# Kernel tuning notes

Measured on AMD Instinct MI355X. Metric: run time of the kernel, lower is better.

The kernel has to match this reference:

```python
import jax, jax.numpy as jnp
import numpy as np

B, M, K = 32768, 8192, 16
EPS = 1e-5  # torch BatchNorm1d default


def _bn_relu(x, g, b):
    # training-mode batch norm (biased variance), matching torch BatchNorm1d forward
    m = x.mean(0)
    v = x.var(0)
    return jax.nn.relu(g * (x - m) * jax.lax.rsqrt(v + EPS) + b)


def _forward(pos, mc, mv, w1, b1, w2, b2, w3, b3, w4, b4, w5, b5, w6, b6,
             g1, be1, g2, be2, g3, be3, g4, be4, g5, be5, k):
    # squared pairwise distances [B, M]; same ordering as L2 norm used by torch.sort
    d2 = (pos * pos).sum(1, keepdims=True) + (mc * mc).sum(1)[None, :] - 2.0 * (pos @ mc.T)
    _, idx = jax.lax.top_k(-d2, k)                     # k nearest indices [B, k]
    nb = jnp.concatenate([mc[idx], mv[idx]], axis=-1)  # [B, k, 4] = (coord, value) per neighbor
    knn_feat = jnp.concatenate([pos, nb.reshape(pos.shape[0], k * 4)], axis=1)  # [B, 2+4k]
    x = _bn_relu(knn_feat @ w1 + b1, g1, be1)
    x = _bn_relu(x @ w2 + b2, g2, be2)
    x = _bn_relu(x @ w3 + b3, g3, be3)
    x = _bn_relu(x @ w4 + b4, g4, be4)
    x = _bn_relu(x @ w5 + b5, g5, be5)  # dropout = identity (eval mode)
    x = x @ w6 + b6
    return x, knn_feat


def setup_inputs() -> dict:
    key = jax.random.key(0)
    ks = jax.random.split(key, 32)
    d_in = 2 + K * 4
    dims = [(d_in, 128), (128, 256), (256, 512), (512, 128), (128, 64), (64, 2)]
    inp = {
        "pos": jax.random.normal(ks[0], (B, 2), jnp.float32),
        "measure_coords": jax.random.normal(ks[1], (M, 2), jnp.float32),
        "measure_vals": jax.random.normal(ks[2], (M, 2), jnp.float32),
    }
    for i, (fi, fo) in enumerate(dims, 1):
        inp[f"w{i}"] = jax.random.normal(ks[2 + 2 * i], (fi, fo), jnp.float32) / np.float32(np.sqrt(fi))
        inp[f"b{i}"] = jnp.zeros((fo,), jnp.float32)
    for i, n in enumerate([128, 256, 512, 128, 64], 1):
        inp[f"g{i}"] = jnp.ones((n,), jnp.float32)
        inp[f"be{i}"] = jnp.zeros((n,), jnp.float32)
    inp["k"] = K
    return inp


def reference(pos, measure_coords, measure_vals, w1, b1, w2, b2, w3, b3, w4, b4,
              w5, b5, w6, b6, g1, be1, g2, be2, g3, be3, g4, be4, g5, be5, k):
    return _forward(pos, measure_coords, measure_vals, w1, b1, w2, b2, w3, b3, w4,
                    b4, w5, b5, w6, b6, g1, be1, g2, be2, g3, be3, g4, be4, g5, be5, k)
```

## Files before the change

### kernel.cpp

```cpp
#include <hip/hip_runtime.h>

typedef unsigned short u16;
typedef unsigned int   u32;
typedef __attribute__((ext_vector_type(8))) short bf16x8;
typedef __attribute__((ext_vector_type(4))) float f32x4;

#define B_ROWS 32768
#define EPS_BN 1e-5f

__device__ __forceinline__ u16 f2bf(float f) {
  u32 u = __float_as_uint(f);
  u32 r = (u + 0x7FFFu + ((u >> 16) & 1u)) >> 16;
  return (u16)r;
}
__device__ __forceinline__ float bf2f(u16 h) {
  return __uint_as_float(((u32)h) << 16);
}

__device__ __forceinline__ float dcalc(float px, float py, float sp, float mx, float my) {
#pragma clang fp contract(off)
  float sm   = mx * mx + my * my;
  float pm   = px * mx;
  float dot  = __builtin_fmaf(py, my, pm);
  float spsm = sp + sm;
  return spsm - 2.0f * dot;
}
__device__ __forceinline__ float dcalc2(float px, float py, float sp, float mx, float my,
                                        float sm) {
#pragma clang fp contract(off)
  float pm   = px * mx;
  float dot  = __builtin_fmaf(py, my, pm);
  float spsm = sp + sm;
  return spsm - 2.0f * dot;
}
__device__ __forceinline__ float smcalc(float mx, float my) {
#pragma clang fp contract(off)
  return mx * mx + my * my;
}
__device__ __forceinline__ float spcalc(float px, float py) {
#pragma clang fp contract(off)
  return px * px + py * py;
}
#define MED3 __builtin_amdgcn_fmed3f

__global__ __launch_bounds__(256, 4)
void knn_kernel(const float2* __restrict__ pos, const float2* __restrict__ mc,
                const float2* __restrict__ mv, float* __restrict__ knn_out,
                u16* __restrict__ X0)
{
  __shared__ float tv[32 * 130];
  __shared__ float tstS[32];
  __shared__ int   qcnt[32];

  const int t = threadIdx.x;
  const int g = t >> 6;
  const int s = t & 63;
  const int q0 = blockIdx.x * 32;

  float px[8], py[8], sp[8];
#pragma unroll
  for (int j = 0; j < 8; ++j) {
    float2 p = pos[q0 + g * 8 + j];
    px[j] = p.x; py[j] = p.y; sp[j] = spcalc(p.x, p.y);
  }

  const float4* mc4 = (const float4*)mc;
  const int b4 = s * 64;
  const int basePt = s * 128;

  float z0[8], z1[8];
#pragma unroll
  for (int j = 0; j < 8; ++j) { z0[j] = __builtin_inff(); z1[j] = __builtin_inff(); }

  float4 cur = mc4[b4];
  for (int i = 0; i < 64; ++i) {
    float4 nxt = mc4[b4 + ((i + 1) & 63)];
    float smA = smcalc(cur.x, cur.y);
    float smB = smcalc(cur.z, cur.w);
#pragma unroll
    for (int j = 0; j < 8; ++j) {
      float dA = dcalc2(px[j], py[j], sp[j], cur.x, cur.y, smA);
      z1[j] = MED3(z0[j], dA, z1[j]); z0[j] = fminf(z0[j], dA);
      float dB = dcalc2(px[j], py[j], sp[j], cur.z, cur.w, smB);
      z1[j] = MED3(z0[j], dB, z1[j]); z0[j] = fminf(z0[j], dB);
    }
    cur = nxt;
  }
#pragma unroll
  for (int j = 0; j < 8; ++j) {
    tv[(g * 8 + j) * 130 + s * 2 + 0] = z0[j];
    tv[(g * 8 + j) * 130 + s * 2 + 1] = z1[j];
  }
  __syncthreads();

  if (t < 32) {
    float ch[16];
#pragma unroll
    for (int j = 0; j < 16; ++j) ch[j] = __builtin_inff();
    for (int k = 0; k < 128; ++k) {
      float v = tv[t * 130 + k];
#pragma unroll
      for (int j = 15; j >= 1; --j) ch[j] = MED3(ch[j-1], v, ch[j]);
      ch[0] = fminf(ch[0], v);
    }
    tstS[t] = ch[15];
    qcnt[t] = 0;
  }
  __syncthreads();
  float Tq[8];
#pragma unroll
  for (int j = 0; j < 8; ++j) Tq[j] = tstS[g * 8 + j];
  __syncthreads();

  u16* qcand = (u16*)tv;
  for (int i = 0; i < 64; ++i) {
    float4 c2 = mc4[b4 + i];
    float smA = smcalc(c2.x, c2.y);
    float smB = smcalc(c2.z, c2.w);
    const int idxA = basePt + 2 * i;
#pragma unroll
    for (int j = 0; j < 8; ++j) {
      float dA = dcalc2(px[j], py[j], sp[j], c2.x, c2.y, smA);
      if (dA <= Tq[j]) {
        int o = atomicAdd(&qcnt[g * 8 + j], 1);
        if (o < 64) qcand[(g * 8 + j) * 64 + o] = (u16)idxA;
      }
      float dB = dcalc2(px[j], py[j], sp[j], c2.z, c2.w, smB);
      if (dB <= Tq[j]) {
        int o = atomicAdd(&qcnt[g * 8 + j], 1);
        if (o < 64) qcand[(g * 8 + j) * 64 + o] = (u16)(idxA + 1);
      }
    }
  }
  __syncthreads();

  if (t < 32) {
    const int q = q0 + t;
    float2 p = pos[q];
    const float sq = spcalc(p.x, p.y);
    int cnt = qcnt[t]; if (cnt > 64) cnt = 64;
    float fd[16]; int fi[16];
#pragma unroll
    for (int j = 0; j < 16; ++j) { fd[j] = __builtin_inff(); fi[j] = 0x7fffffff; }
    for (int j = 0; j < cnt; ++j) {
      int ci = qcand[t * 64 + j];
      float2 m = mc[ci];
      float d = dcalc(p.x, p.y, sq, m.x, m.y);
      bool cc = (d < fd[15]) || (d == fd[15] && ci < fi[15]);
      if (cc) {
#pragma unroll
        for (int k = 15; k >= 1; --k) {
          bool cm = (d < fd[k-1]) || (d == fd[k-1] && ci < fi[k-1]);
          if (cc) {
            if (cm) { fd[k] = fd[k-1]; fi[k] = fi[k-1]; }
            else    { fd[k] = d;       fi[k] = ci;      }
          }
          cc = cm;
        }
        if (cc) { fd[0] = d; fi[0] = ci; }
      }
    }
    float* orow = knn_out + (size_t)q * 66;
    u16*   xrow = X0 + (size_t)q * 96;
    orow[0] = p.x; orow[1] = p.y;
    xrow[0] = f2bf(p.x); xrow[1] = f2bf(p.y);
#pragma unroll
    for (int j = 0; j < 16; ++j) {
      int ci = fi[j];
      float2 m = mc[ci], v = mv[ci];
      orow[2 + 4*j + 0] = m.x; orow[2 + 4*j + 1] = m.y;
      orow[2 + 4*j + 2] = v.x; orow[2 + 4*j + 3] = v.y;
      xrow[2 + 4*j + 0] = f2bf(m.x); xrow[2 + 4*j + 1] = f2bf(m.y);
      xrow[2 + 4*j + 2] = f2bf(v.x); xrow[2 + 4*j + 3] = f2bf(v.y);
    }
#pragma unroll
    for (int c = 66; c < 96; ++c) xrow[c] = 0;
  }
}

__global__ __launch_bounds__(256)
void prep_wt_all(const float* __restrict__ w1, const float* __restrict__ w2,
                 const float* __restrict__ w3, const float* __restrict__ w4,
                 const float* __restrict__ w5,
                 u16* __restrict__ wt1, u16* __restrict__ wt2, u16* __restrict__ wt3,
                 u16* __restrict__ wt4, u16* __restrict__ wt5)
{
  const int l = blockIdx.y;
  const float* w; u16* wt; int K, N, Kp;
  if (l == 0)      { w = w1; wt = wt1; K = 66;  N = 128; Kp = 96;  }
  else if (l == 1) { w = w2; wt = wt2; K = 128; N = 256; Kp = 128; }
  else if (l == 2) { w = w3; wt = wt3; K = 256; N = 512; Kp = 256; }
  else if (l == 3) { w = w4; wt = wt4; K = 512; N = 128; Kp = 512; }
  else             { w = w5; wt = wt5; K = 128; N = 64;  Kp = 128; }
  int i = blockIdx.x * 256 + threadIdx.x;
  if (i >= N * Kp) return;
  int n = i / Kp, kp = i - n * Kp;
  float v = (kp < K) ? w[(size_t)kp * N + n] : 0.0f;
  wt[i] = f2bf(v);
}

template<int BN, bool FUSE>
__global__ __launch_bounds__(256)
void gemm_bn_kernel(const u16* __restrict__ X, int Kw,
                    const u16* __restrict__ WT,
                    const float* __restrict__ bias,
                    const float* __restrict__ psum, const float* __restrict__ psq,
                    const float* __restrict__ gw,   const float* __restrict__ bw,
                    u16* __restrict__ Z, int N,
                    float* __restrict__ csum, float* __restrict__ csq)
{
  constexpr int BM = 128;
  constexpr int AST = 40;
  __shared__ u16 Ash[BM * AST];
  __shared__ u16 Bsh[BN * AST];
  __shared__ float redS[4][BN];
  __shared__ float redQ[4][BN];
  __shared__ float scA[512];
  __shared__ float ttA[512];

  const int t = threadIdx.x;
  const int wave = t >> 6;
  const int lane = t & 63;
  const int lr = lane & 15;
  const int qd = lane >> 4;
  const int m0 = blockIdx.x * BM;
  const int n0 = blockIdx.y * BN;

  if (FUSE) {
    const float invB = 1.0f / 32768.0f;
    for (int c = t; c < Kw; c += 256) {
      float mean = psum[c] * invB;
      float var  = __fmaf_rn(-mean, mean, psq[c] * invB);
      float sc   = gw[c] * rsqrtf(var + EPS_BN);
      scA[c] = sc;
      ttA[c] = __fmaf_rn(-mean, sc, bw[c]);
    }
    __syncthreads();
  }

  f32x4 acc[2][BN / 16];
#pragma unroll
  for (int a = 0; a < 2; ++a)
#pragma unroll
    for (int b = 0; b < BN / 16; ++b) {
      acc[a][b][0] = 0.f; acc[a][b][1] = 0.f; acc[a][b][2] = 0.f; acc[a][b][3] = 0.f;
    }

  const int sr = t >> 2;
  const int sk = (t & 3) * 8;

  for (int k0 = 0; k0 < Kw; k0 += 32) {
#pragma unroll
    for (int rr = 0; rr < 2; ++rr) {
      int r = sr + rr * 64;
      uint4 g = *(const uint4*)(&X[(size_t)(m0 + r) * Kw + k0 + sk]);
      if (FUSE) {
        u32 w[4] = {g.x, g.y, g.z, g.w};
        u32 o[4];
#pragma unroll
        for (int e = 0; e < 4; ++e) {
          int kk = k0 + sk + 2 * e;
          float lo = bf2f((u16)(w[e] & 0xffffu));
          float hi = bf2f((u16)(w[e] >> 16));
          float yl = fmaxf(__fmaf_rn(lo, scA[kk],     ttA[kk]),     0.0f);
          float yh = fmaxf(__fmaf_rn(hi, scA[kk + 1], ttA[kk + 1]), 0.0f);
          o[e] = (u32)f2bf(yl) | ((u32)f2bf(yh) << 16);
        }
        g.x = o[0]; g.y = o[1]; g.z = o[2]; g.w = o[3];
      }
      *(uint4*)(&Ash[r * AST + sk]) = g;
    }
    if (BN == 128) {
#pragma unroll
      for (int rr = 0; rr < 2; ++rr) {
        int n = sr + rr * 64;
        *(uint4*)(&Bsh[n * AST + sk]) =
            *(const uint4*)(&WT[(size_t)(n0 + n) * Kw + k0 + sk]);
      }
    } else {
      int n = sr;
      *(uint4*)(&Bsh[n * AST + sk]) =
          *(const uint4*)(&WT[(size_t)(n0 + n) * Kw + k0 + sk]);
    }
    __syncthreads();
    bf16x8 af0 = *(const bf16x8*)(&Ash[(wave * 32 + lr) * AST + qd * 8]);
    bf16x8 af1 = *(const bf16x8*)(&Ash[(wave * 32 + 16 + lr) * AST + qd * 8]);
#pragma unroll
    for (int ct = 0; ct < BN / 16; ++ct) {
      bf16x8 bfr = *(const bf16x8*)(&Bsh[(ct * 16 + lr) * AST + qd * 8]);
      acc[0][ct] = __builtin_amdgcn_mfma_f32_16x16x32_bf16(af0, bfr, acc[0][ct], 0, 0, 0);
      acc[1][ct] = __builtin_amdgcn_mfma_f32_16x16x32_bf16(af1, bfr, acc[1][ct], 0, 0, 0);
    }
    __syncthreads();
  }

#pragma unroll
  for (int ct = 0; ct < BN / 16; ++ct) {
    int cg = n0 + ct * 16 + lr;
    float bv = bias[cg];
    float s = 0.f, sqv = 0.f;
#pragma unroll
    for (int rt = 0; rt < 2; ++rt) {
#pragma unroll
      for (int r = 0; r < 4; ++r) {
        float z = acc[rt][ct][r] + bv;
        int row = m0 + wave * 32 + rt * 16 + qd * 4 + r;
        Z[(size_t)row * N + cg] = f2bf(z);
        s += z;
        sqv = __fmaf_rn(z, z, sqv);
      }
    }
    s   += __shfl_xor(s, 16);   s   += __shfl_xor(s, 32);
    sqv += __shfl_xor(sqv, 16); sqv += __shfl_xor(sqv, 32);
    if (qd == 0) { redS[wave][ct * 16 + lr] = s; redQ[wave][ct * 16 + lr] = sqv; }
  }
  __syncthreads();
  if (t < BN) {
    float s  = redS[0][t] + redS[1][t] + redS[2][t] + redS[3][t];
    float sv = redQ[0][t] + redQ[1][t] + redQ[2][t] + redQ[3][t];
    atomicAdd(&csum[n0 + t], s);
    atomicAdd(&csq[n0 + t], sv);
  }
}

__global__ __launch_bounds__(256)
void gemv6_kernel(const u16* __restrict__ Z5, const float* __restrict__ w6,
                  const float* __restrict__ b6,
                  const float* __restrict__ psum, const float* __restrict__ psq,
                  const float* __restrict__ gw,   const float* __restrict__ bw,
                  float* __restrict__ out)
{
  __shared__ float wsh[128];
  __shared__ float scs[64];
  __shared__ float tts[64];
  const int t = threadIdx.x;
  if (t < 128) wsh[t] = w6[t];
  if (t < 64) {
    const float invB = 1.0f / 32768.0f;
    float mean = psum[t] * invB;
    float var  = __fmaf_rn(-mean, mean, psq[t] * invB);
    float sc   = gw[t] * rsqrtf(var + EPS_BN);
    scs[t] = sc;
    tts[t] = __fmaf_rn(-mean, sc, bw[t]);
  }
  __syncthreads();
  const int q = blockIdx.x * 256 + t;
  const uint4* xv = (const uint4*)(Z5 + (size_t)q * 64);
  float a0 = 0.f, a1 = 0.f;
#pragma unroll
  for (int cc = 0; cc < 8; ++cc) {
    uint4 pk = xv[cc];
    u32 u[4] = {pk.x, pk.y, pk.z, pk.w};
#pragma unroll
    for (int uu = 0; uu < 4; ++uu) {
      int k = cc * 8 + uu * 2;
      float z0 = bf2f((u16)(u[uu] & 0xffffu));
      float z1 = bf2f((u16)(u[uu] >> 16));
      float x0 = fmaxf(__fmaf_rn(z0, scs[k],     tts[k]),     0.0f);
      float x1 = fmaxf(__fmaf_rn(z1, scs[k + 1], tts[k + 1]), 0.0f);
      x0 = bf2f(f2bf(x0));
      x1 = bf2f(f2bf(x1));
      a0 = __fmaf_rn(x0, wsh[2 * k + 0], a0);
      a1 = __fmaf_rn(x0, wsh[2 * k + 1], a1);
      a0 = __fmaf_rn(x1, wsh[2 * k + 2], a0);
      a1 = __fmaf_rn(x1, wsh[2 * k + 3], a1);
    }
  }
  float2 o; o.x = a0 + b6[0]; o.y = a1 + b6[1];
  ((float2*)out)[q] = o;
}

extern "C" void kernel_launch(void* const* d_in, const int* in_sizes, int n_in,
                              void* d_out, int out_size, void* d_ws, size_t ws_size,
                              hipStream_t stream)
{
  const float2* pos = (const float2*)d_in[0];
  const float2* mc  = (const float2*)d_in[1];
  const float2* mv  = (const float2*)d_in[2];
  const float* w1 = (const float*)d_in[3];  const float* b1 = (const float*)d_in[4];
  const float* w2 = (const float*)d_in[5];  const float* b2 = (const float*)d_in[6];
  const float* w3 = (const float*)d_in[7];  const float* b3 = (const float*)d_in[8];
  const float* w4 = (const float*)d_in[9];  const float* b4 = (const float*)d_in[10];
  const float* w5 = (const float*)d_in[11]; const float* b5 = (const float*)d_in[12];
  const float* w6 = (const float*)d_in[13]; const float* b6 = (const float*)d_in[14];
  const float* g1 = (const float*)d_in[15]; const float* be1 = (const float*)d_in[16];
  const float* g2 = (const float*)d_in[17]; const float* be2 = (const float*)d_in[18];
  const float* g3 = (const float*)d_in[19]; const float* be3 = (const float*)d_in[20];
  const float* g4 = (const float*)d_in[21]; const float* be4 = (const float*)d_in[22];
  const float* g5 = (const float*)d_in[23]; const float* be5 = (const float*)d_in[24];

  char* ws = (char*)d_ws;
  u16* X0   = (u16*)(ws + 0);
  u16* ZA   = (u16*)(ws + 6291456);
  u16* ZB   = (u16*)(ws + 39845888);
  u16* WT1  = (u16*)(ws + 73400320);
  u16* WT2  = (u16*)(ws + 73424896);
  u16* WT3  = (u16*)(ws + 73490432);
  u16* WT4  = (u16*)(ws + 73752576);
  u16* WT5  = (u16*)(ws + 73883648);
  float* stats = (float*)(ws + 73900032);
  float* s1 = stats;        float* s2 = stats + 128;  float* s3 = stats + 384;
  float* s4 = stats + 896;  float* s5 = stats + 1024;
  float* sqb = stats + 1088;
  float* q1 = sqb;          float* q2 = sqb + 128;    float* q3 = sqb + 384;
  float* q4 = sqb + 896;    float* q5 = sqb + 1024;

  float* outX = (float*)d_out;
  float* outK = outX + 2 * B_ROWS;

  hipMemsetAsync(stats, 0, 2176 * sizeof(float), stream);
  prep_wt_all<<<dim3(512, 5), 256, 0, stream>>>(w1, w2, w3, w4, w5, WT1, WT2, WT3, WT4, WT5);
  knn_kernel<<<dim3(1024), 256, 0, stream>>>(pos, mc, mv, outK, X0);

  gemm_bn_kernel<64, false><<<dim3(256, 2), 256, 0, stream>>>(
      X0, 96, WT1, b1, nullptr, nullptr, nullptr, nullptr, ZA, 128, s1, q1);
  gemm_bn_kernel<64, true><<<dim3(256, 4), 256, 0, stream>>>(
      ZA, 128, WT2, b2, s1, q1, g1, be1, ZB, 256, s2, q2);
  gemm_bn_kernel<64, true><<<dim3(256, 8), 256, 0, stream>>>(
      ZB, 256, WT3, b3, s2, q2, g2, be2, ZA, 512, s3, q3);
  gemm_bn_kernel<64, true><<<dim3(256, 2), 256, 0, stream>>>(
      ZA, 512, WT4, b4, s3, q3, g3, be3, ZB, 128, s4, q4);
  gemm_bn_kernel<64, true><<<dim3(256, 1), 256, 0, stream>>>(
      ZB, 128, WT5, b5, s4, q4, g4, be4, ZA, 64, s5, q5);
  gemv6_kernel<<<dim3(128), 256, 0, stream>>>(ZA, w6, b6, s5, q5, g5, be5, outX);

  (void)in_sizes; (void)n_in; (void)out_size; (void)ws_size;
}
```

Measured before the change: 360.1 us.

## Rescan only slices whose local min passes the threshold, compacted via ballot

The second candidate-collection pass no longer rescans every slice of measurement points for every query. A ballot over each lane's local minimum marks only the (query, slice) pairs that can hold a point under the top-k threshold, and those pairs are spread across lanes to be rescanned. This cuts the redundant distance evaluations and atomics in the second pass, at the cost of bit-select and per-lane branching work. Separately, the distance formula now uses an explicit fma for the final term, which may change rounding relative to the reference ordering.

```diff
diff --git a/kernel.cpp b/kernel.cpp
--- a/kernel.cpp
+++ b/kernel.cpp
@@ -23,7 +23,7 @@
   float pm   = px * mx;
   float dot  = __builtin_fmaf(py, my, pm);
   float spsm = sp + sm;
-  return spsm - 2.0f * dot;
+  return __builtin_fmaf(dot, -2.0f, spsm);
 }
 __device__ __forceinline__ float dcalc2(float px, float py, float sp, float mx, float my,
                                         float sm) {
@@ -31,7 +31,7 @@
   float pm   = px * mx;
   float dot  = __builtin_fmaf(py, my, pm);
   float spsm = sp + sm;
-  return spsm - 2.0f * dot;
+  return __builtin_fmaf(dot, -2.0f, spsm);
 }
 __device__ __forceinline__ float smcalc(float mx, float my) {
 #pragma clang fp contract(off)
@@ -42,6 +42,29 @@
   return px * px + py * py;
 }
 #define MED3 __builtin_amdgcn_fmed3f
+
+__device__ __forceinline__ int nth_set_bit(unsigned long long m, int n) {
+  u32 w = (u32)m;
+  int base = 0;
+  int c = __popc(w);
+  if (n >= c) { n -= c; w = (u32)(m >> 32); base = 32; }
+  int p = __popc(w & 0xFFFFu); if (n >= p) { n -= p; w >>= 16; base += 16; }
+  p = __popc(w & 0xFFu);       if (n >= p) { n -= p; w >>= 8;  base += 8; }
+  p = __popc(w & 0xFu);        if (n >= p) { n -= p; w >>= 4;  base += 4; }
+  p = __popc(w & 0x3u);        if (n >= p) { n -= p; w >>= 2;  base += 2; }
+  p = (int)(w & 1u);           if (n >= p) { base += 1; }
+  return base;
+}
+
+__device__ __forceinline__ float sel8(const float a[8], int j) {
+  float x01 = (j & 1) ? a[1] : a[0];
+  float x23 = (j & 1) ? a[3] : a[2];
+  float x45 = (j & 1) ? a[5] : a[4];
+  float x67 = (j & 1) ? a[7] : a[6];
+  float xl  = (j & 2) ? x23 : x01;
+  float xh  = (j & 2) ? x67 : x45;
+  return (j & 4) ? xh : xl;
+}
 
 __global__ __launch_bounds__(256, 4)
 void knn_kernel(const float2* __restrict__ pos, const float2* __restrict__ mc,
@@ -66,7 +89,6 @@
 
   const float4* mc4 = (const float4*)mc;
   const int b4 = s * 64;
-  const int basePt = s * 128;
 
   float z0[8], z1[8];
 #pragma unroll
@@ -88,8 +110,8 @@
   }
 #pragma unroll
   for (int j = 0; j < 8; ++j) {
-    tv[(g * 8 + j) * 130 + s * 2 + 0] = z0[j];
-    tv[(g * 8 + j) * 130 + s * 2 + 1] = z1[j];
+    float2 zz; zz.x = z0[j]; zz.y = z1[j];
+    *(float2*)(&tv[(g * 8 + j) * 130 + s * 2]) = zz;
   }
   __syncthreads();
 
@@ -112,23 +134,43 @@
   for (int j = 0; j < 8; ++j) Tq[j] = tstS[g * 8 + j];
   __syncthreads();
 
+  unsigned long long am[8];
+#pragma unroll
+  for (int j = 0; j < 8; ++j) am[j] = __ballot(z0[j] <= Tq[j]);
+  int total = 0;
+#pragma unroll
+  for (int j = 0; j < 8; ++j) total += __popcll(am[j]);
+
   u16* qcand = (u16*)tv;
-  for (int i = 0; i < 64; ++i) {
-    float4 c2 = mc4[b4 + i];
-    float smA = smcalc(c2.x, c2.y);
-    float smB = smcalc(c2.z, c2.w);
-    const int idxA = basePt + 2 * i;
-#pragma unroll
-    for (int j = 0; j < 8; ++j) {
-      float dA = dcalc2(px[j], py[j], sp[j], c2.x, c2.y, smA);
-      if (dA <= Tq[j]) {
-        int o = atomicAdd(&qcnt[g * 8 + j], 1);
-        if (o < 64) qcand[(g * 8 + j) * 64 + o] = (u16)idxA;
-      }
-      float dB = dcalc2(px[j], py[j], sp[j], c2.z, c2.w, smB);
-      if (dB <= Tq[j]) {
-        int o = atomicAdd(&qcnt[g * 8 + j], 1);
-        if (o < 64) qcand[(g * 8 + j) * 64 + o] = (u16)(idxA + 1);
+  for (int t0 = s; t0 < total; t0 += 64) {
+    int rem = t0, jq = 0, sl = -1;
+#pragma unroll
+    for (int jj = 0; jj < 8; ++jj) {
+      if (sl < 0) {
+        int c = __popcll(am[jj]);
+        if (rem < c) { sl = nth_set_bit(am[jj], rem); jq = jj; }
+        else rem -= c;
+      }
+    }
+    float qx = sel8(px, jq), qy = sel8(py, jq);
+    float qs = sel8(sp, jq), qT = sel8(Tq, jq);
+    const int qrow = g * 8 + jq;
+    const int bpt = sl * 128;
+    const float4* mbase = mc4 + sl * 64;
+#pragma unroll 4
+    for (int i = 0; i < 64; ++i) {
+      float4 c2 = mbase[i];
+      float smA = smcalc(c2.x, c2.y);
+      float smB = smcalc(c2.z, c2.w);
+      float dA = dcalc2(qx, qy, qs, c2.x, c2.y, smA);
+      float dB = dcalc2(qx, qy, qs, c2.z, c2.w, smB);
+      if (dA <= qT) {
+        int o = atomicAdd(&qcnt[qrow], 1);
+        if (o < 64) qcand[qrow * 64 + o] = (u16)(bpt + 2 * i);
+      }
+      if (dB <= qT) {
+        int o = atomicAdd(&qcnt[qrow], 1);
+        if (o < 64) qcand[qrow * 64 + o] = (u16)(bpt + 2 * i + 1);
       }
     }
   }
```

Result: no change. 354.3 us (-1.6%).
